# Performance work log

Measured on AMD Instinct MI355X. Metric: run time of the kernel, lower is better.

Reference implementation:

```python
import jax, jax.numpy as jnp
import numpy as np

B, H, O = 16384, 1024, 512


def setup_inputs() -> dict:
    key = jax.random.key(0)
    ks = jax.random.split(key, 8)
    s = 1.0 / np.sqrt(H)  # PyTorch-style uniform init scale (values only matter for numerics)
    return {
        "inp": jax.random.normal(ks[0], (B, O), jnp.float32),
        "hidden": jax.random.normal(ks[1], (1, B, H), jnp.float32),
        "w_ih": jax.random.uniform(ks[2], (3 * H, O), jnp.float32, -s, s),
        "w_hh": jax.random.uniform(ks[3], (3 * H, H), jnp.float32, -s, s),
        "b_ih": jax.random.uniform(ks[4], (3 * H,), jnp.float32, -s, s),
        "b_hh": jax.random.uniform(ks[5], (3 * H,), jnp.float32, -s, s),
        "w_out": jax.random.uniform(ks[6], (O, H), jnp.float32, -s, s),
        "b_out": jax.random.uniform(ks[7], (O,), jnp.float32, -s, s),
    }


def reference(inp, hidden, w_ih, w_hh, b_ih, b_hh, w_out, b_out):
    # Single-step GRU (PyTorch gate order r, z, n) + Linear + tanh.
    h = hidden[0]                                # [B, H]
    gi = inp @ w_ih.T + b_ih                     # [B, 3H]
    gh = h @ w_hh.T + b_hh                       # [B, 3H]
    i_r, i_z, i_n = jnp.split(gi, 3, axis=-1)
    h_r, h_z, h_n = jnp.split(gh, 3, axis=-1)
    r = jax.nn.sigmoid(i_r + h_r)
    z = jax.nn.sigmoid(i_z + h_z)
    n = jnp.tanh(i_n + r * h_n)
    h_new = (1.0 - z) * n + z * h                # [B, H]
    out = jnp.tanh(h_new @ w_out.T + b_out)      # [B, O]
    return out, h_new[None]                      # hidden back to [1, B, H]
```

## Files before the change

### kernel.cpp

```cpp
#include <hip/hip_runtime.h>

typedef __bf16 bf16x8 __attribute__((ext_vector_type(8)));
typedef float  f32x4  __attribute__((ext_vector_type(4)));
typedef unsigned short us8 __attribute__((ext_vector_type(8)));

__device__ __forceinline__ unsigned short f2bf(float f) {
  unsigned int u = __builtin_bit_cast(unsigned int, f);
  u += 0x7FFFu + ((u >> 16) & 1u);
  return (unsigned short)(u >> 16);
}
__device__ __forceinline__ float sigmoid_f(float x) {
  return 1.f / (1.f + __expf(-x));
}
__device__ __forceinline__ float tanh_f(float x) {
  float e = __expf(2.f * x);
  return 1.f - 2.f / (e + 1.f);
}

__device__ __forceinline__ void relayout_region(
    const float* __restrict__ srcRowBase, size_t rowStride,
    unsigned short* __restrict__ dst, float* __restrict__ lp, int lane) {
  {
    int r = lane >> 2, c = (lane & 3) << 3;
    const float* s = srcRowBase + (size_t)r * rowStride + c;
    f32x4 a = *(const f32x4*)(s);
    f32x4 b = *(const f32x4*)(s + 4);
#pragma unroll
    for (int j = 0; j < 4; ++j) { lp[r * 33 + c + j] = a[j]; lp[r * 33 + c + 4 + j] = b[j]; }
  }
  int s4 = lane >> 4, r16 = lane & 15;
  us8 o;
#pragma unroll
  for (int j = 0; j < 8; ++j) o[j] = f2bf(lp[r16 * 33 + s4 * 8 + j]);
  *(us8*)(dst + lane * 8) = o;
}

__global__ __launch_bounds__(256) void prep_all(
    const float* __restrict__ inp, const float* __restrict__ hidden,
    const float* __restrict__ w_ih, const float* __restrict__ w_hh,
    const float* __restrict__ w_out,
    unsigned short* __restrict__ inp_r, unsigned short* __restrict__ h_r,
    unsigned short* __restrict__ wih_r, unsigned short* __restrict__ whh_r,
    unsigned short* __restrict__ wout_r)
{
  __shared__ float lp[4][16 * 33];
  const int wIn = threadIdx.x >> 6, lane = threadIdx.x & 63;
  const int gw  = blockIdx.x * 4 + wIn;

  const float* src; unsigned short* dst; int K, local, isA;
  if      (gw < 2048) { src = inp;    dst = inp_r;  K = 512;  isA = 1; local = gw; }
  else if (gw < 6144) { src = hidden; dst = h_r;    K = 1024; isA = 1; local = gw - 2048; }
  else if (gw < 6912) { src = w_ih;   dst = wih_r;  K = 512;  isA = 0; local = gw - 6144; }
  else if (gw < 8448) { src = w_hh;   dst = whh_r;  K = 1024; isA = 0; local = gw - 6912; }
  else                { src = w_out;  dst = wout_r; K = 1024; isA = 1; local = gw - 8448; }
  const int nkt = K >> 5;

  if (isA) {
    int p = local / nkt, kt = local - p * nkt;
    const float* base = src + (size_t)p * 128 * K + kt * 32;
    unsigned short* d = dst + (size_t)local * 4096;
#pragma unroll
    for (int g = 0; g < 8; ++g)
      relayout_region(base + (size_t)g * 16 * K, K, d + g * 512, lp[wIn], lane);
  } else {
    int qg = local / nkt, kt = local - qg * nkt;
    int q = qg / 3, g = qg - q * 3;
    const float* base = src + ((size_t)g * 1024 + q * 64) * K + kt * 32;
    unsigned short* d = dst + (size_t)local * 2048;
#pragma unroll
    for (int rg = 0; rg < 4; ++rg)
      relayout_region(base + (size_t)rg * 16 * K, K, d + rg * 512, lp[wIn], lane);
  }
}

#define GLOAD(gp, lp) __builtin_amdgcn_global_load_lds( \
    (const __attribute__((address_space(1))) unsigned int*)(gp), \
    (__attribute__((address_space(3))) unsigned int*)(lp), 16, 0, 0)

__global__ __launch_bounds__(256, 2) void fused_gru(
    const unsigned short* __restrict__ inp_r,
    const unsigned short* __restrict__ h_r,
    const unsigned short* __restrict__ wih_r,
    const unsigned short* __restrict__ whh_r,
    const float* __restrict__ b_ih,
    const float* __restrict__ b_hh,
    const float* __restrict__ hidden,
    float* __restrict__ hnew_f32,
    unsigned short* __restrict__ hnew_img)
{
  __shared__ unsigned short ls[4][10240];

  const int tid  = threadIdx.x;
  const int lane = tid & 63;
  const int wave = tid >> 6;
  const int wr = wave >> 1, wc = wave & 1;

  const int f  = blockIdx.y * 16 + blockIdx.x;
  const int bx = ((f & 7) << 1) | ((f >> 3) & 1);
  const int by = f >> 4;

  f32x4 accR[4][2], accZ[4][2], accNi[4][2], accNh[4][2];
#pragma unroll
  for (int m = 0; m < 4; ++m)
#pragma unroll
    for (int n = 0; n < 2; ++n) {
      accR[m][n]  = f32x4{0.f, 0.f, 0.f, 0.f};
      accZ[m][n]  = f32x4{0.f, 0.f, 0.f, 0.f};
      accNi[m][n] = f32x4{0.f, 0.f, 0.f, 0.f};
      accNh[m][n] = f32x4{0.f, 0.f, 0.f, 0.f};
    }

  const int t4   = lane >> 4;
  const int l15  = lane & 15;
  const int rofs = t4 * 128 + l15 * 8;

  const unsigned short* aptr = inp_r + (size_t)by * (16 * 4096);
  const unsigned short* wptr = wih_r + (size_t)bx * (3 * 16 * 2048);
  int wgs = 16 * 2048;

#define STAGE(BUF) do { \
    GLOAD(aptr + tid * 8,           &ls[BUF][tid * 8]); \
    GLOAD(aptr + 2048 + tid * 8,    &ls[BUF][2048 + tid * 8]); \
    GLOAD(wptr + tid * 8,           &ls[BUF][4096 + tid * 8]); \
    GLOAD(wptr + wgs + tid * 8,     &ls[BUF][6144 + tid * 8]); \
    GLOAD(wptr + 2 * wgs + tid * 8, &ls[BUF][8192 + tid * 8]); \
    aptr += 4096; wptr += 2048; \
  } while (0)

#define COMPUTE(BUF, ACCN) do { \
    const unsigned short* lb = &ls[BUF][0]; \
    bf16x8 af[4], bfr[3][2]; \
    _Pragma("unroll") for (int m = 0; m < 4; ++m) \
      af[m] = *(const bf16x8*)&lb[(wr * 4 + m) * 512 + rofs]; \
    _Pragma("unroll") for (int g = 0; g < 3; ++g) { \
      _Pragma("unroll") for (int n = 0; n < 2; ++n) \
        bfr[g][n] = *(const bf16x8*)&lb[4096 + g * 2048 + (wc * 2 + n) * 512 + rofs]; \
    } \
    __builtin_amdgcn_s_setprio(1); \
    _Pragma("unroll") for (int m = 0; m < 4; ++m) { \
      _Pragma("unroll") for (int n = 0; n < 2; ++n) { \
        accR[m][n] = __builtin_amdgcn_mfma_f32_16x16x32_bf16(af[m], bfr[0][n], accR[m][n], 0, 0, 0); \
        accZ[m][n] = __builtin_amdgcn_mfma_f32_16x16x32_bf16(af[m], bfr[1][n], accZ[m][n], 0, 0, 0); \
        ACCN[m][n] = __builtin_amdgcn_mfma_f32_16x16x32_bf16(af[m], bfr[2][n], ACCN[m][n], 0, 0, 0); \
      } \
    } \
    __builtin_amdgcn_s_setprio(0); \
  } while (0)

#define WAIT10 asm volatile("s_waitcnt vmcnt(10)" ::: "memory")
#define BARR   __builtin_amdgcn_s_barrier()
#define STEP(SB, CB, ACCN) do { STAGE(SB); WAIT10; BARR; COMPUTE(CB, ACCN); } while (0)

  STAGE(0); STAGE(1);
#pragma unroll 1
  for (int i = 0; i < 3; ++i) {
    STEP(2, 0, accNi); STEP(3, 1, accNi); STEP(0, 2, accNi); STEP(1, 3, accNi);
  }
  STEP(2, 0, accNi);
  STEP(3, 1, accNi);
  aptr = h_r + (size_t)by * (32 * 4096);
  wptr = whh_r + (size_t)bx * (3 * 32 * 2048);
  wgs = 32 * 2048;
  STEP(0, 2, accNi);
  STEP(1, 3, accNi);
#pragma unroll 1
  for (int i = 0; i < 7; ++i) {
    STEP(2, 0, accNh); STEP(3, 1, accNh); STEP(0, 2, accNh); STEP(1, 3, accNh);
  }
  STEP(2, 0, accNh);
  STEP(3, 1, accNh);
  asm volatile("s_waitcnt vmcnt(5)" ::: "memory"); BARR;
  COMPUTE(2, accNh);
  asm volatile("s_waitcnt vmcnt(0)" ::: "memory"); BARR;
  COMPUTE(3, accNh);

#undef STAGE
#undef COMPUTE
#undef WAIT10
#undef BARR
#undef STEP

  const int m0 = by * 128;
  const int n0 = bx * 64;
  const int colb = n0 + wc * 32 + l15;
  const int rowb = m0 + wr * 64 + (t4 << 2);
#pragma unroll
  for (int n = 0; n < 2; ++n) {
    int c = colb + n * 16;
    float br  = b_ih[c]        + b_hh[c];
    float bz  = b_ih[1024 + c] + b_hh[1024 + c];
    float bni = b_ih[2048 + c];
    float bnh = b_hh[2048 + c];
    const int kt = c >> 5;
    const int s  = (c >> 3) & 3;
    const int e  = c & 7;
#pragma unroll
    for (int m = 0; m < 4; ++m) {
      int row = rowb + m * 16;
#pragma unroll
      for (int r = 0; r < 4; ++r) {
        float rg = sigmoid_f(accR[m][n][r] + br);
        float zg = sigmoid_f(accZ[m][n][r] + bz);
        float ng = tanh_f((accNi[m][n][r] + bni) + rg * (accNh[m][n][r] + bnh));
        int rw = row + r;
        float ho = hidden[(size_t)rw * 1024 + c];
        float hv = (1.f - zg) * ng + zg * ho;
        hnew_f32[(size_t)rw * 1024 + c] = hv;
        size_t img = ((size_t)((rw >> 7) * 32 + kt)) * 4096
                   + (((rw >> 4) & 7) * 512) + s * 128 + (rw & 15) * 8 + e;
        hnew_img[img] = f2bf(hv);
      }
    }
  }
}

__global__ __launch_bounds__(256, 2) void gemm_out(
    const unsigned short* __restrict__ A_img,
    const unsigned short* __restrict__ B_img,
    float* __restrict__ Cout,
    const float* __restrict__ bias)
{
  __shared__ unsigned short ls[4][8192];

  const int tid  = threadIdx.x;
  const int lane = tid & 63;
  const int wave = tid >> 6;
  const int wr = wave >> 1, wc = wave & 1;

  f32x4 acc[4][4];
#pragma unroll
  for (int i = 0; i < 4; ++i)
#pragma unroll
    for (int j = 0; j < 4; ++j) acc[i][j] = f32x4{0.f, 0.f, 0.f, 0.f};

  const int t4   = lane >> 4;
  const int l15  = lane & 15;
  const int rofs = t4 * 128 + l15 * 8;

  const unsigned short* aptr = A_img + (size_t)blockIdx.y * (32 * 4096);
  const unsigned short* bptr = B_img + (size_t)blockIdx.x * (32 * 4096);

#define STAGE(BUF) do { \
    GLOAD(aptr + tid * 8,        &ls[BUF][tid * 8]); \
    GLOAD(aptr + 2048 + tid * 8, &ls[BUF][2048 + tid * 8]); \
    GLOAD(bptr + tid * 8,        &ls[BUF][4096 + tid * 8]); \
    GLOAD(bptr + 2048 + tid * 8, &ls[BUF][6144 + tid * 8]); \
    aptr += 4096; bptr += 4096; \
  } while (0)

#define COMPUTE(BUF) do { \
    const unsigned short* lb = &ls[BUF][0]; \
    bf16x8 af[4], bfr[4]; \
    _Pragma("unroll") for (int m = 0; m < 4; ++m) \
      af[m] = *(const bf16x8*)&lb[(wr * 4 + m) * 512 + rofs]; \
    _Pragma("unroll") for (int n = 0; n < 4; ++n) \
      bfr[n] = *(const bf16x8*)&lb[4096 + (wc * 4 + n) * 512 + rofs]; \
    __builtin_amdgcn_s_setprio(1); \
    _Pragma("unroll") for (int m = 0; m < 4; ++m) { \
      _Pragma("unroll") for (int n = 0; n < 4; ++n) \
        acc[m][n] = __builtin_amdgcn_mfma_f32_16x16x32_bf16(af[m], bfr[n], acc[m][n], 0, 0, 0); \
    } \
    __builtin_amdgcn_s_setprio(0); \
  } while (0)

#define WAIT8 asm volatile("s_waitcnt vmcnt(8)" ::: "memory")
#define BARR  __builtin_amdgcn_s_barrier()
#define STEP(SB, CB) do { STAGE(SB); WAIT8; BARR; COMPUTE(CB); } while (0)

  STAGE(0); STAGE(1);
#pragma unroll 1
  for (int i = 0; i < 7; ++i) {
    STEP(2, 0); STEP(3, 1); STEP(0, 2); STEP(1, 3);
  }
  STEP(2, 0);
  STEP(3, 1);
  asm volatile("s_waitcnt vmcnt(4)" ::: "memory"); BARR;
  COMPUTE(2);
  asm volatile("s_waitcnt vmcnt(0)" ::: "memory"); BARR;
  COMPUTE(3);

#undef STAGE
#undef COMPUTE
#undef WAIT8
#undef BARR
#undef STEP

  const int m0 = blockIdx.y * 128;
  const int n0 = blockIdx.x * 128;
  const int colb = n0 + wc * 64 + l15;
  const int rowb = m0 + wr * 64 + (t4 << 2);
#pragma unroll
  for (int n = 0; n < 4; ++n) {
    int col = colb + n * 16;
    float bv = bias[col];
#pragma unroll
    for (int m = 0; m < 4; ++m) {
      int row = rowb + m * 16;
#pragma unroll
      for (int r = 0; r < 4; ++r) {
        Cout[(size_t)(row + r) * 512 + col] = tanh_f(acc[m][n][r] + bv);
      }
    }
  }
}

extern "C" void kernel_launch(void* const* d_in, const int* in_sizes, int n_in,
                              void* d_out, int out_size, void* d_ws, size_t ws_size,
                              hipStream_t stream) {
  const int B = 16384, H = 1024, O = 512;
  const float* inp    = (const float*)d_in[0];
  const float* hidden = (const float*)d_in[1];
  const float* w_ih   = (const float*)d_in[2];
  const float* w_hh   = (const float*)d_in[3];
  const float* b_ih   = (const float*)d_in[4];
  const float* b_hh   = (const float*)d_in[5];
  const float* w_out  = (const float*)d_in[6];
  const float* b_out  = (const float*)d_in[7];

  float* out      = (float*)d_out;
  float* hnew_out = out + (size_t)B * O;

  char* ws = (char*)d_ws;
  size_t need = 0;
  auto carve = [&](size_t elems) {
    unsigned short* p = (unsigned short*)(ws + need);
    need += elems * 2;
    return p;
  };
  unsigned short* inp_r  = carve((size_t)B * O);
  unsigned short* h_r    = carve((size_t)B * H);
  unsigned short* wih_r  = carve((size_t)3 * H * O);
  unsigned short* whh_r  = carve((size_t)3 * H * H);
  unsigned short* wout_r = carve((size_t)O * H);
  unsigned short* hnew_i = carve((size_t)B * H);
  if (ws_size < need) return;

  prep_all<<<dim3(2144), dim3(256), 0, stream>>>(
      inp, hidden, w_ih, w_hh, w_out, inp_r, h_r, wih_r, whh_r, wout_r);

  fused_gru<<<dim3(H / 64, B / 128), dim3(256), 0, stream>>>(
      inp_r, h_r, wih_r, whh_r, b_ih, b_hh, hidden, hnew_out, hnew_i);

  gemm_out<<<dim3(O / 128, B / 128), dim3(256), 0, stream>>>(
      hnew_i, wout_r, out, b_out);
}
```

Measured before the change: 219.4 us.

## Switch GEMM K-loop to double-buffered 64-wide K stages

Replaces the four-slot, 32-wide K ring buffer with two LDS buffers that each hold a 64-wide K slice (two 32-wide sub-steps) and issue ten async global-to-LDS loads per stage. This halves the number of barrier/wait steps per K element and amortises sync overhead, but adds a second barrier per step and reduces prefetch depth to one stage ahead. The intent is lower synchronisation cost in the fused GRU gate GEMM, at the risk of exposing more load latency.

```diff
diff --git a/kernel.cpp b/kernel.cpp
--- a/kernel.cpp
+++ b/kernel.cpp
@@ -88,7 +88,7 @@
     float* __restrict__ hnew_f32,
     unsigned short* __restrict__ hnew_img)
 {
-  __shared__ unsigned short ls[4][10240];
+  __shared__ unsigned short ls[2][20480];
 
   const int tid  = threadIdx.x;
   const int lane = tid & 63;
@@ -115,26 +115,33 @@
   const int rofs = t4 * 128 + l15 * 8;
 
   const unsigned short* aptr = inp_r + (size_t)by * (16 * 4096);
-  const unsigned short* wptr = wih_r + (size_t)bx * (3 * 16 * 2048);
-  int wgs = 16 * 2048;
+  const unsigned short* w0   = wih_r + (size_t)bx * (3 * 16 * 2048);
+  const unsigned short* w1   = w0 + 16 * 2048;
+  const unsigned short* w2   = w1 + 16 * 2048;
 
 #define STAGE(BUF) do { \
-    GLOAD(aptr + tid * 8,           &ls[BUF][tid * 8]); \
-    GLOAD(aptr + 2048 + tid * 8,    &ls[BUF][2048 + tid * 8]); \
-    GLOAD(wptr + tid * 8,           &ls[BUF][4096 + tid * 8]); \
-    GLOAD(wptr + wgs + tid * 8,     &ls[BUF][6144 + tid * 8]); \
-    GLOAD(wptr + 2 * wgs + tid * 8, &ls[BUF][8192 + tid * 8]); \
-    aptr += 4096; wptr += 2048; \
+    GLOAD(aptr + tid * 8,        &ls[BUF][tid * 8]); \
+    GLOAD(aptr + 2048 + tid * 8, &ls[BUF][2048 + tid * 8]); \
+    GLOAD(aptr + 4096 + tid * 8, &ls[BUF][4096 + tid * 8]); \
+    GLOAD(aptr + 6144 + tid * 8, &ls[BUF][6144 + tid * 8]); \
+    GLOAD(w0 + tid * 8,          &ls[BUF][8192 + tid * 8]); \
+    GLOAD(w0 + 2048 + tid * 8,   &ls[BUF][10240 + tid * 8]); \
+    GLOAD(w1 + tid * 8,          &ls[BUF][12288 + tid * 8]); \
+    GLOAD(w1 + 2048 + tid * 8,   &ls[BUF][14336 + tid * 8]); \
+    GLOAD(w2 + tid * 8,          &ls[BUF][16384 + tid * 8]); \
+    GLOAD(w2 + 2048 + tid * 8,   &ls[BUF][18432 + tid * 8]); \
+    aptr += 8192; w0 += 4096; w1 += 4096; w2 += 4096; \
   } while (0)
 
-#define COMPUTE(BUF, ACCN) do { \
-    const unsigned short* lb = &ls[BUF][0]; \
+#define COMPUTE(BUF, KS, ACCN) do { \
+    const unsigned short* la = &ls[BUF][(KS) * 4096]; \
+    const unsigned short* lw = &ls[BUF][8192 + (KS) * 2048]; \
     bf16x8 af[4], bfr[3][2]; \
     _Pragma("unroll") for (int m = 0; m < 4; ++m) \
-      af[m] = *(const bf16x8*)&lb[(wr * 4 + m) * 512 + rofs]; \
+      af[m] = *(const bf16x8*)&la[(wr * 4 + m) * 512 + rofs]; \
     _Pragma("unroll") for (int g = 0; g < 3; ++g) { \
       _Pragma("unroll") for (int n = 0; n < 2; ++n) \
-        bfr[g][n] = *(const bf16x8*)&lb[4096 + g * 2048 + (wc * 2 + n) * 512 + rofs]; \
+        bfr[g][n] = *(const bf16x8*)&lw[g * 4096 + (wc * 2 + n) * 512 + rofs]; \
     } \
     __builtin_amdgcn_s_setprio(1); \
     _Pragma("unroll") for (int m = 0; m < 4; ++m) { \
@@ -148,35 +155,34 @@
   } while (0)
 
 #define WAIT10 asm volatile("s_waitcnt vmcnt(10)" ::: "memory")
+#define WAIT0  asm volatile("s_waitcnt vmcnt(0)" ::: "memory")
 #define BARR   __builtin_amdgcn_s_barrier()
-#define STEP(SB, CB, ACCN) do { STAGE(SB); WAIT10; BARR; COMPUTE(CB, ACCN); } while (0)
-
-  STAGE(0); STAGE(1);
+#define STEP(SB, CB, ACCN) do { STAGE(SB); WAIT10; BARR; \
+    COMPUTE(CB, 0, ACCN); COMPUTE(CB, 1, ACCN); BARR; } while (0)
+
+  STAGE(0);
 #pragma unroll 1
   for (int i = 0; i < 3; ++i) {
-    STEP(2, 0, accNi); STEP(3, 1, accNi); STEP(0, 2, accNi); STEP(1, 3, accNi);
-  }
-  STEP(2, 0, accNi);
-  STEP(3, 1, accNi);
+    STEP(1, 0, accNi); STEP(0, 1, accNi);
+  }
+  STEP(1, 0, accNi);
   aptr = h_r + (size_t)by * (32 * 4096);
-  wptr = whh_r + (size_t)bx * (3 * 32 * 2048);
-  wgs = 32 * 2048;
-  STEP(0, 2, accNi);
-  STEP(1, 3, accNi);
+  w0 = whh_r + (size_t)bx * (3 * 32 * 2048);
+  w1 = w0 + 32 * 2048;
+  w2 = w1 + 32 * 2048;
+  STEP(0, 1, accNi);
 #pragma unroll 1
   for (int i = 0; i < 7; ++i) {
-    STEP(2, 0, accNh); STEP(3, 1, accNh); STEP(0, 2, accNh); STEP(1, 3, accNh);
-  }
-  STEP(2, 0, accNh);
-  STEP(3, 1, accNh);
-  asm volatile("s_waitcnt vmcnt(5)" ::: "memory"); BARR;
-  COMPUTE(2, accNh);
-  asm volatile("s_waitcnt vmcnt(0)" ::: "memory"); BARR;
-  COMPUTE(3, accNh);
+    STEP(1, 0, accNh); STEP(0, 1, accNh);
+  }
+  STEP(1, 0, accNh);
+  WAIT0; BARR;
+  COMPUTE(1, 0, accNh); COMPUTE(1, 1, accNh);
 
 #undef STAGE
 #undef COMPUTE
 #undef WAIT10
+#undef WAIT0
 #undef BARR
 #undef STEP
 
```

Measured after the change: 226.2 us. 3.1% more time.
